# Optimization experiments

Measured on AMD Instinct MI355X. Metric: run time of the kernel, lower is better.

## Reference

```python
import jax, jax.numpy as jnp
import numpy as np

FCM_ITERS = 3
FCM_M = 2.0
EPS = 1e-8


def batched_index_select(x, idx):
    # x: [B, C, M, 1], idx: [B, N, K] -> [B, C, N, K]
    xt = x[..., 0]  # [B, C, M]
    return jnp.take_along_axis(xt[:, :, None, :], idx[:, None, :, :], axis=3)


def fcm_centroids(x, num_clusters):
    # Fuzzy c-means soft clustering (HyperedgeConstruction).
    # x: [B, C, N, 1] -> centroids [B, C, K], weights [B, N, 1, K]
    xt = jnp.transpose(x[..., 0], (0, 2, 1))  # [B, N, C]
    B, N, C = xt.shape
    init_idx = jnp.linspace(0, N - 1, num_clusters).astype(jnp.int32)
    cent = xt[:, init_idx, :]  # [B, K, C] deterministic init
    expo = -1.0 / (FCM_M - 1.0)

    def memberships(cent):
        xn = jnp.sum(xt * xt, axis=-1)            # [B, N]
        cn = jnp.sum(cent * cent, axis=-1)        # [B, K]
        d2 = xn[:, :, None] + cn[:, None, :] - 2.0 * jnp.einsum('bnc,bkc->bnk', xt, cent)
        d2 = jnp.maximum(d2, EPS)
        inv = d2 ** expo
        return inv / jnp.sum(inv, axis=-1, keepdims=True)  # [B, N, K]

    for _ in range(FCM_ITERS):
        u = memberships(cent)
        um = u ** FCM_M
        cent = jnp.einsum('bnk,bnc->bkc', um, xt) / (jnp.sum(um, axis=1)[..., None] + EPS)
    u = memberships(cent)
    centroids = jnp.transpose(cent, (0, 2, 1))  # [B, C, K]
    return centroids, u[:, :, None, :]          # weights [B, N, 1, K]


def setup_inputs() -> dict:
    key = jax.random.key(0)
    k1, k2, k3, k4 = jax.random.split(key, 4)
    B, C, N, K = 4, 64, 8192, 16
    OC = 64
    return {
        "x": jax.random.normal(k1, (B, C, N, 1), jnp.float32),
        "edge_index": jax.random.randint(k2, (2, B, N, K), 0, N),
        "W": jax.random.normal(k3, (OC, 3 * C), jnp.float32) / np.sqrt(3 * C).astype(np.float32),
        "b": jax.random.normal(k4, (OC,), jnp.float32) * 0.01,
        "num_clusters": 50,
        "top_clusters": 5,
    }


def reference(x, edge_index, W, b, num_clusters, top_clusters):
    B, C, N, _ = x.shape
    # max-relative neighbor feature
    x_i = batched_index_select(x, edge_index[1])          # [B, C, N, K]
    x_j = batched_index_select(x, edge_index[0])          # [B, C, N, K]
    x_j = jnp.max(x_j - x_i, axis=-1, keepdims=True)      # [B, C, N, 1]
    # soft-cluster (hyperedge) feature
    centroids, weights = fcm_centroids(x, num_clusters)   # [B,C,K], [B,N,1,K]
    weights = weights[:, :, 0, :]                         # squeeze(-2) -> [B, N, K]
    _, nn_idx_centroid = jax.lax.top_k(weights, top_clusters)  # [B, N, top]
    x_j_cluster = batched_index_select(centroids[..., None], nn_idx_centroid)  # [B, C, N, top]
    # x gathered at center_idx == x broadcast over top dim
    x_j_cluster = jnp.max(x_j_cluster - x, axis=-1, keepdims=True)  # [B, C, N, 1]
    # interleaved concat: [B, C, 3, N, 1] -> [B, 3C, N, 1]
    feat = jnp.stack([x, x_j, x_j_cluster], axis=2).reshape(B, 3 * C, N, 1)
    # BasicConv: 1x1 conv + ReLU
    out = jnp.einsum('oc,bcni->boni', W, feat) + b[None, :, None, None]
    return jax.nn.relu(out)
```

## Files before the change

kernel.cpp:

```cpp
#include <hip/hip_runtime.h>


constexpr int B  = 4;
constexpr int C  = 64;
constexpr int N  = 8192;
constexpr int KE = 16;
constexpr int OC = 64;
constexpr int NC = 50;
constexpr int TC = 5;
constexpr int C3 = 192;
constexpr int KG  = 5;
constexpr int NKG = 10;
constexpr int NS  = 8;
constexpr int MW  = 16;
constexpr float FEPS = 1e-8f;

__global__ __launch_bounds__(256) void k_transpose(const float* __restrict__ x,
                                                   float* __restrict__ xt,
                                                   float* __restrict__ xn) {
  __shared__ float tile[64][65];
  int b  = blockIdx.x >> 7;
  int n0 = (blockIdx.x & 127) << 6;
  int tid = threadIdx.x;
  int nl = tid & 63, cq = tid >> 6;
#pragma unroll
  for (int r = 0; r < 16; ++r) {
    int cc = r * 4 + cq;
    tile[cc][nl] = x[((size_t)b * C + cc) * N + n0 + nl];
  }
  __syncthreads();
  int cl = tid & 63, nq = tid >> 6;
#pragma unroll
  for (int r = 0; r < 16; ++r) {
    int nr = r * 4 + nq;
    xt[((size_t)b * N + n0 + nr) * C + cl] = tile[cl][nr];
  }
  if (tid < 64) {
    float s = 0.f;
#pragma unroll
    for (int cc = 0; cc < 64; ++cc) { float v = tile[cc][tid]; s = fmaf(v, v, s); }
    xn[(size_t)b * N + n0 + tid] = s;
  }
}

__global__ __launch_bounds__(256) void k_init(const float* __restrict__ xt,
                                              float* __restrict__ cent,
                                              float* __restrict__ cn) {
  int i = blockIdx.x * 256 + threadIdx.x;
  int lane = threadIdx.x & 63;
  int ccol = i & 63;
  int row  = i >> 6;
  int k = row % NC, b = row / NC;
  int src = (k * (N - 1)) / (NC - 1);
  float v = xt[((size_t)b * N + src) * C + ccol];
  cent[i] = v;
  float sq = v * v;
#pragma unroll
  for (int off = 32; off; off >>= 1) sq += __shfl_down(sq, off, 64);
  if (lane == 0) cn[row] = sq;
}

__global__ __launch_bounds__(512) void k_m1(const float* __restrict__ xt,
                                            const float* __restrict__ xn,
                                            const float* __restrict__ cent,
                                            const float* __restrict__ cn,
                                            float* __restrict__ umT) {
  int gid = blockIdx.x;
  int xcd = gid & 7;
  int b = xcd >> 1;
  int chunk = ((gid >> 3) << 1) + (xcd & 1);
  int n0 = chunk << 6;
  int w = __builtin_amdgcn_readfirstlane((int)threadIdx.x >> 6);
  int lane = threadIdx.x & 63;
  int n = n0 + lane;
  int base = (w < 2) ? 7 * w : 14 + 6 * (w - 2);
  int cnt  = (w < 2) ? 7 : 6;
  const float* xr = xt + ((size_t)b * N + n) * C;
  const float* cb = cent + b * NC * C;
  float dot[7];
#pragma unroll
  for (int j = 0; j < 7; ++j) dot[j] = 0.f;
  for (int c4 = 0; c4 < C; c4 += 4) {
    float4 xv = *(const float4*)(xr + c4);
#pragma unroll
    for (int j = 0; j < 7; ++j) {
      int kk = base + j; kk = (kk < NC) ? kk : 0;
      float4 cv = *(const float4*)(cb + kk * C + c4);
      dot[j] = fmaf(xv.x, cv.x, dot[j]);
      dot[j] = fmaf(xv.y, cv.y, dot[j]);
      dot[j] = fmaf(xv.z, cv.z, dot[j]);
      dot[j] = fmaf(xv.w, cv.w, dot[j]);
    }
  }
  float xnv = xn[(size_t)b * N + n];
  const float* cnb = cn + b * NC;
  float inv[7];
  float psum = 0.f;
#pragma unroll
  for (int j = 0; j < 7; ++j) {
    int kk = base + j; kk = (kk < NC) ? kk : 0;
    float d2 = fmaf(-2.f, dot[j], xnv + cnb[kk]);
    d2 = fmaxf(d2, FEPS);
    float iv = 1.f / d2;
    inv[j] = iv;
    psum += (j < cnt) ? iv : 0.f;
  }
  __shared__ float s_ps[8][64];
  s_ps[w][lane] = psum;
  __syncthreads();
  float ssum = 0.f;
#pragma unroll
  for (int ww = 0; ww < 8; ++ww) ssum += s_ps[ww][lane];
  float s2i = 1.f / (ssum * ssum);
  float* upT = umT + ((size_t)b * NC + base) * N + n;
#pragma unroll
  for (int j = 0; j < 7; ++j)
    if (j < cnt) upT[(size_t)j * N] = inv[j] * inv[j] * s2i;
}

__global__ __launch_bounds__(1024) void k_m2(const float* __restrict__ umT,
                                             const float* __restrict__ xt,
                                             float* __restrict__ part_c,
                                             float* __restrict__ part_u) {
  int gid = blockIdx.x;
  int xcd = gid & 7;
  int b = xcd >> 1;
  int r = ((gid >> 3) << 1) + (xcd & 1);
  int kg = r >> 3;
  int s  = r & 7;
  int k0 = kg * KG;
  int w = __builtin_amdgcn_readfirstlane((int)threadIdx.x >> 6);
  int c = threadIdx.x & 63;
  int sn0 = s * (N / NS);
  int nb = w * 64;
  const float* uT = umT + ((size_t)b * NC + k0) * N + sn0 + nb;
  const float* xb = xt + ((size_t)(b * N + sn0 + nb)) * C + c;
  float acc[KG], ua[KG];
#pragma unroll
  for (int j = 0; j < KG; ++j) { acc[j] = 0.f; ua[j] = 0.f; }
  for (int n4 = 0; n4 < 64; n4 += 4) {
    float4 u4[KG];
#pragma unroll
    for (int j = 0; j < KG; ++j)
      u4[j] = *(const float4*)(uT + (size_t)j * N + n4);
#pragma unroll
    for (int t = 0; t < 4; ++t) {
      float xv = xb[(size_t)(n4 + t) * C];
#pragma unroll
      for (int j = 0; j < KG; ++j) {
        float u = (t == 0) ? u4[j].x : (t == 1) ? u4[j].y : (t == 2) ? u4[j].z : u4[j].w;
        acc[j] = fmaf(u, xv, acc[j]);
        ua[j] += u;
      }
    }
  }
  __shared__ float s_acc[MW][KG][64];
  __shared__ float s_ua[MW][KG];
#pragma unroll
  for (int j = 0; j < KG; ++j) s_acc[w][j][c] = acc[j];
  if (c == 0) {
#pragma unroll
    for (int j = 0; j < KG; ++j) s_ua[w][j] = ua[j];
  }
  __syncthreads();
  if (w == 0) {
#pragma unroll
    for (int j = 0; j < KG; ++j) {
      float t = 0.f;
#pragma unroll
      for (int ww = 0; ww < MW; ++ww) t += s_acc[ww][j][c];
      part_c[((size_t)s * (B * NC) + b * NC + k0 + j) * C + c] = t;
    }
    if (c == 0) {
#pragma unroll
      for (int j = 0; j < KG; ++j) {
        float t = 0.f;
#pragma unroll
        for (int ww = 0; ww < MW; ++ww) t += s_ua[ww][j];
        part_u[(size_t)s * (B * NC) + b * NC + k0 + j] = t;
      }
    }
  }
}

__global__ __launch_bounds__(256) void k_m3(const float* __restrict__ part_c,
                                            const float* __restrict__ part_u,
                                            float* __restrict__ cent,
                                            float* __restrict__ cn) {
  int i = blockIdx.x * 256 + threadIdx.x;
  int lane = threadIdx.x & 63;
  int row = i >> 6;
  float tot = 0.f;
#pragma unroll
  for (int s = 0; s < NS; ++s) tot += part_c[(size_t)s * (B * NC * C) + i];
  float us = 0.f;
#pragma unroll
  for (int s = 0; s < NS; ++s) us += part_u[(size_t)s * (B * NC) + row];
  float v = tot / (us + FEPS);
  cent[i] = v;
  float sq = v * v;
#pragma unroll
  for (int off = 32; off; off >>= 1) sq += __shfl_down(sq, off, 64);
  if (lane == 0) cn[row] = sq;
}

__global__ __launch_bounds__(512) void k_top5(const float* __restrict__ xt,
                                              const float* __restrict__ xn,
                                              const float* __restrict__ cent,
                                              const float* __restrict__ cn,
                                              int* __restrict__ t5) {
  int gid = blockIdx.x;
  int xcd = gid & 7;
  int b = xcd >> 1;
  int chunk = ((gid >> 3) << 1) + (xcd & 1);
  int n0 = chunk << 6;
  int w = __builtin_amdgcn_readfirstlane((int)threadIdx.x >> 6);
  int lane = threadIdx.x & 63;
  int n = n0 + lane;
  int base = (w < 2) ? 7 * w : 14 + 6 * (w - 2);
  int cnt  = (w < 2) ? 7 : 6;
  const float* xr = xt + ((size_t)b * N + n) * C;
  const float* cb = cent + b * NC * C;
  float dot[7];
#pragma unroll
  for (int j = 0; j < 7; ++j) dot[j] = 0.f;
  for (int c4 = 0; c4 < C; c4 += 4) {
    float4 xv = *(const float4*)(xr + c4);
#pragma unroll
    for (int j = 0; j < 7; ++j) {
      int kk = base + j; kk = (kk < NC) ? kk : 0;
      float4 cv = *(const float4*)(cb + kk * C + c4);
      dot[j] = fmaf(xv.x, cv.x, dot[j]);
      dot[j] = fmaf(xv.y, cv.y, dot[j]);
      dot[j] = fmaf(xv.z, cv.z, dot[j]);
      dot[j] = fmaf(xv.w, cv.w, dot[j]);
    }
  }
  float xnv = xn[(size_t)b * N + n];
  const float* cnb = cn + b * NC;
  __shared__ float s_inv[NC][65];
#pragma unroll
  for (int j = 0; j < 7; ++j) {
    int kk = base + j; kk = (kk < NC) ? kk : 0;
    float d2 = fmaxf(fmaf(-2.f, dot[j], xnv + cnb[kk]), FEPS);
    float iv = 1.f / d2;
    if (j < cnt) s_inv[base + j][lane] = iv;
  }
  __syncthreads();
  if (w == 0) {
    float v[NC];
#pragma unroll
    for (int k = 0; k < NC; ++k) v[k] = s_inv[k][lane];
    unsigned long long taken = 0ull;
    int* tp = t5 + ((size_t)b * N + n) * TC;
#pragma unroll
    for (int t = 0; t < TC; ++t) {
      float best = -1.f;
      int bi = 0;
#pragma unroll
      for (int k = 0; k < NC; ++k) {
        bool ok = (((taken >> k) & 1ull) == 0ull) && (v[k] > best);
        best = ok ? v[k] : best;
        bi   = ok ? k : bi;
      }
      taken |= (1ull << bi);
      tp[t] = bi;
    }
  }
}

__global__ __launch_bounds__(512, 4) void k_out(const float* __restrict__ xt,
                                                const float* __restrict__ cent,
                                                const float* __restrict__ W,
                                                const int* __restrict__ t5,
                                                const int* __restrict__ eidx,
                                                const float* __restrict__ bias,
                                                float* __restrict__ out) {
  __shared__ float s_feat[C3][65];
  int tid = threadIdx.x;
  int gid = blockIdx.x;
  int xcd = gid & 7;
  int b = xcd >> 1;
  int chunk = ((gid >> 3) << 1) + (xcd & 1);
  int wv = __builtin_amdgcn_readfirstlane(tid >> 6);
  int lane = tid & 63;
  int n0 = chunk * 64;
  int nw0 = n0 + wv * 8;
  const float* xtb = xt + ((size_t)b * N) * C;
  const float* cb  = cent + b * NC * C;
  const int* e0b = eidx + ((size_t)b * N) * KE;
  const int* e1b = eidx + ((size_t)(B + b) * N) * KE;
  int c = lane;
  int fr = wv * 8;
#pragma unroll
  for (int j = 0; j < 8; ++j) {
    int n = nw0 + j;
    const int* p0 = e0b + (size_t)n * KE;
    const int* p1 = e1b + (size_t)n * KE;
    const int* tp = t5 + ((size_t)b * N + n) * TC;
    float x0 = xtb[(size_t)n * C + c];
    float g0[KE], g1[KE];
#pragma unroll
    for (int k = 0; k < KE; ++k) {
      g0[k] = xtb[(size_t)p0[k] * C + c];
      g1[k] = xtb[(size_t)p1[k] * C + c];
    }
    float cv[TC];
#pragma unroll
    for (int t = 0; t < TC; ++t) cv[t] = cb[(size_t)tp[t] * C + c];
    float m1 = g0[0] - g1[0];
#pragma unroll
    for (int k = 1; k < KE; ++k) m1 = fmaxf(m1, g0[k] - g1[k]);
    float cm = cv[0];
#pragma unroll
    for (int t = 1; t < TC; ++t) cm = fmaxf(cm, cv[t]);
    s_feat[3 * c + 0][fr + j] = x0;
    s_feat[3 * c + 1][fr + j] = m1;
    s_feat[3 * c + 2][fr + j] = cm - x0;
  }
  __syncthreads();
  int o0 = wv * 8;
  float acc[8];
#pragma unroll
  for (int oj = 0; oj < 8; ++oj) acc[oj] = bias[o0 + oj];
#pragma unroll 4
  for (int f = 0; f < C3; ++f) {
    float v = s_feat[f][lane];
#pragma unroll
    for (int oj = 0; oj < 8; ++oj)
      acc[oj] = fmaf(W[(size_t)(o0 + oj) * C3 + f], v, acc[oj]);
  }
  float* ob = out + ((size_t)b * OC + o0) * N + n0 + lane;
#pragma unroll
  for (int oj = 0; oj < 8; ++oj)
    ob[(size_t)oj * N] = fmaxf(acc[oj], 0.f);
}

extern "C" void kernel_launch(void* const* d_in, const int* in_sizes, int n_in,
                              void* d_out, int out_size, void* d_ws, size_t ws_size,
                              hipStream_t stream) {
  const float* x    = (const float*)d_in[0];
  const int*   eidx = (const int*)d_in[1];
  const float* W    = (const float*)d_in[2];
  const float* bias = (const float*)d_in[3];

  float* ws   = (float*)d_ws;
  float* xt   = ws;
  float* xn   = xt + (size_t)B * N * C;
  float* cent = xn + (size_t)B * N;
  float* cn   = cent + B * NC * C;
  float* umT  = cn + 256;
  float* pc   = umT + (size_t)B * NC * N;
  float* pu   = pc + (size_t)NS * B * NC * C;
  int*   t5   = (int*)(pu + NS * B * NC);
  float* out  = (float*)d_out;

  k_transpose<<<dim3(B * (N / 64)), dim3(256), 0, stream>>>(x, xt, xn);
  k_init<<<dim3((B * NC * C) / 256), dim3(256), 0, stream>>>(xt, cent, cn);
  for (int it = 0; it < 3; ++it) {
    k_m1<<<dim3(512), dim3(512), 0, stream>>>(xt, xn, cent, cn, umT);
    k_m2<<<dim3(B * NKG * NS), dim3(1024), 0, stream>>>(umT, xt, pc, pu);
    k_m3<<<dim3((B * NC * C) / 256), dim3(256), 0, stream>>>(pc, pu, cent, cn);
  }
  k_top5<<<dim3(512), dim3(512), 0, stream>>>(xt, xn, cent, cn, t5);
  k_out<<<dim3(512), dim3(512), 0, stream>>>(xt, cent, W, t5, eidx, bias, out);
}
```

Before: 240.9 us.

## Fuse FCM membership and centroid partial-sum kernels via shared memory

Merges the membership kernel and the centroid accumulation kernel into one kernel per iteration. Each block keeps its 64-point slice of features and the membership values in shared memory and writes per-chunk partial centroid sums directly. This removes the global write and re-read of the B×NC×N membership matrix and one launch per iteration. In exchange the final reduction kernel now sums 128 partial slices instead of 8, and the accumulation loop reads shared memory with possible bank conflicts.

```diff
diff --git a/kernel.cpp b/kernel.cpp
--- a/kernel.cpp
+++ b/kernel.cpp
@@ -9,10 +9,7 @@
 constexpr int NC = 50;
 constexpr int TC = 5;
 constexpr int C3 = 192;
-constexpr int KG  = 5;
-constexpr int NKG = 10;
-constexpr int NS  = 8;
-constexpr int MW  = 16;
+constexpr int NSL = 128;
 constexpr float FEPS = 1e-8f;
 
 __global__ __launch_bounds__(256) void k_transpose(const float* __restrict__ x,
@@ -60,11 +57,15 @@
   if (lane == 0) cn[row] = sq;
 }
 
-__global__ __launch_bounds__(512) void k_m1(const float* __restrict__ xt,
-                                            const float* __restrict__ xn,
-                                            const float* __restrict__ cent,
-                                            const float* __restrict__ cn,
-                                            float* __restrict__ umT) {
+__global__ __launch_bounds__(512) void k_fcm(const float* __restrict__ xt,
+                                             const float* __restrict__ xn,
+                                             const float* __restrict__ cent,
+                                             const float* __restrict__ cn,
+                                             float* __restrict__ pc,
+                                             float* __restrict__ pu) {
+  __shared__ float s_xt[64][68];
+  __shared__ float s_u[NC][64];
+  __shared__ float s_ps[8][64];
   int gid = blockIdx.x;
   int xcd = gid & 7;
   int b = xcd >> 1;
@@ -82,6 +83,7 @@
   for (int j = 0; j < 7; ++j) dot[j] = 0.f;
   for (int c4 = 0; c4 < C; c4 += 4) {
     float4 xv = *(const float4*)(xr + c4);
+    if (w == 0) *(float4*)(&s_xt[lane][c4]) = xv;
 #pragma unroll
     for (int j = 0; j < 7; ++j) {
       int kk = base + j; kk = (kk < NC) ? kk : 0;
@@ -105,97 +107,54 @@
     inv[j] = iv;
     psum += (j < cnt) ? iv : 0.f;
   }
-  __shared__ float s_ps[8][64];
   s_ps[w][lane] = psum;
   __syncthreads();
   float ssum = 0.f;
 #pragma unroll
   for (int ww = 0; ww < 8; ++ww) ssum += s_ps[ww][lane];
   float s2i = 1.f / (ssum * ssum);
-  float* upT = umT + ((size_t)b * NC + base) * N + n;
 #pragma unroll
   for (int j = 0; j < 7; ++j)
-    if (j < cnt) upT[(size_t)j * N] = inv[j] * inv[j] * s2i;
-}
-
-__global__ __launch_bounds__(1024) void k_m2(const float* __restrict__ umT,
-                                             const float* __restrict__ xt,
-                                             float* __restrict__ part_c,
-                                             float* __restrict__ part_u) {
-  int gid = blockIdx.x;
-  int xcd = gid & 7;
-  int b = xcd >> 1;
-  int r = ((gid >> 3) << 1) + (xcd & 1);
-  int kg = r >> 3;
-  int s  = r & 7;
-  int k0 = kg * KG;
-  int w = __builtin_amdgcn_readfirstlane((int)threadIdx.x >> 6);
-  int c = threadIdx.x & 63;
-  int sn0 = s * (N / NS);
-  int nb = w * 64;
-  const float* uT = umT + ((size_t)b * NC + k0) * N + sn0 + nb;
-  const float* xb = xt + ((size_t)(b * N + sn0 + nb)) * C + c;
-  float acc[KG], ua[KG];
-#pragma unroll
-  for (int j = 0; j < KG; ++j) { acc[j] = 0.f; ua[j] = 0.f; }
-  for (int n4 = 0; n4 < 64; n4 += 4) {
-    float4 u4[KG];
-#pragma unroll
-    for (int j = 0; j < KG; ++j)
-      u4[j] = *(const float4*)(uT + (size_t)j * N + n4);
-#pragma unroll
-    for (int t = 0; t < 4; ++t) {
-      float xv = xb[(size_t)(n4 + t) * C];
-#pragma unroll
-      for (int j = 0; j < KG; ++j) {
-        float u = (t == 0) ? u4[j].x : (t == 1) ? u4[j].y : (t == 2) ? u4[j].z : u4[j].w;
-        acc[j] = fmaf(u, xv, acc[j]);
-        ua[j] += u;
-      }
-    }
-  }
-  __shared__ float s_acc[MW][KG][64];
-  __shared__ float s_ua[MW][KG];
-#pragma unroll
-  for (int j = 0; j < KG; ++j) s_acc[w][j][c] = acc[j];
-  if (c == 0) {
-#pragma unroll
-    for (int j = 0; j < KG; ++j) s_ua[w][j] = ua[j];
-  }
-  __syncthreads();
-  if (w == 0) {
-#pragma unroll
-    for (int j = 0; j < KG; ++j) {
-      float t = 0.f;
-#pragma unroll
-      for (int ww = 0; ww < MW; ++ww) t += s_acc[ww][j][c];
-      part_c[((size_t)s * (B * NC) + b * NC + k0 + j) * C + c] = t;
-    }
-    if (c == 0) {
-#pragma unroll
-      for (int j = 0; j < KG; ++j) {
-        float t = 0.f;
-#pragma unroll
-        for (int ww = 0; ww < MW; ++ww) t += s_ua[ww][j];
-        part_u[(size_t)s * (B * NC) + b * NC + k0 + j] = t;
-      }
-    }
-  }
-}
-
-__global__ __launch_bounds__(256) void k_m3(const float* __restrict__ part_c,
-                                            const float* __restrict__ part_u,
+    if (j < cnt) s_u[base + j][lane] = inv[j] * inv[j] * s2i;
+  __syncthreads();
+  int c = lane;
+  float acc[7], ua[7];
+#pragma unroll
+  for (int j = 0; j < 7; ++j) { acc[j] = 0.f; ua[j] = 0.f; }
+  for (int nn = 0; nn < 64; ++nn) {
+    float xv = s_xt[nn][c];
+#pragma unroll
+    for (int j = 0; j < 7; ++j) {
+      int kk = base + j; kk = (kk < NC) ? kk : 0;
+      float u = s_u[kk][nn];
+      acc[j] = fmaf(u, xv, acc[j]);
+      ua[j] += u;
+    }
+  }
+  float* pcb = pc + (((size_t)chunk * (B * NC) + b * NC + base)) * C + c;
+#pragma unroll
+  for (int j = 0; j < 7; ++j)
+    if (j < cnt) pcb[(size_t)j * C] = acc[j];
+  if (lane == 0) {
+#pragma unroll
+    for (int j = 0; j < 7; ++j)
+      if (j < cnt) pu[(size_t)chunk * (B * NC) + b * NC + base + j] = ua[j];
+  }
+}
+
+__global__ __launch_bounds__(256) void k_m3(const float* __restrict__ pc,
+                                            const float* __restrict__ pu,
                                             float* __restrict__ cent,
                                             float* __restrict__ cn) {
   int i = blockIdx.x * 256 + threadIdx.x;
   int lane = threadIdx.x & 63;
   int row = i >> 6;
   float tot = 0.f;
-#pragma unroll
-  for (int s = 0; s < NS; ++s) tot += part_c[(size_t)s * (B * NC * C) + i];
+#pragma unroll 16
+  for (int s = 0; s < NSL; ++s) tot += pc[(size_t)s * (B * NC * C) + i];
   float us = 0.f;
-#pragma unroll
-  for (int s = 0; s < NS; ++s) us += part_u[(size_t)s * (B * NC) + row];
+#pragma unroll 16
+  for (int s = 0; s < NSL; ++s) us += pu[(size_t)s * (B * NC) + row];
   float v = tot / (us + FEPS);
   cent[i] = v;
   float sq = v * v;
@@ -349,17 +308,15 @@
   float* xn   = xt + (size_t)B * N * C;
   float* cent = xn + (size_t)B * N;
   float* cn   = cent + B * NC * C;
-  float* umT  = cn + 256;
-  float* pc   = umT + (size_t)B * NC * N;
-  float* pu   = pc + (size_t)NS * B * NC * C;
-  int*   t5   = (int*)(pu + NS * B * NC);
+  float* pc   = cn + 256;
+  float* pu   = pc + (size_t)NSL * B * NC * C;
+  int*   t5   = (int*)(pu + (size_t)NSL * B * NC);
   float* out  = (float*)d_out;
 
   k_transpose<<<dim3(B * (N / 64)), dim3(256), 0, stream>>>(x, xt, xn);
   k_init<<<dim3((B * NC * C) / 256), dim3(256), 0, stream>>>(xt, cent, cn);
   for (int it = 0; it < 3; ++it) {
-    k_m1<<<dim3(512), dim3(512), 0, stream>>>(xt, xn, cent, cn, umT);
-    k_m2<<<dim3(B * NKG * NS), dim3(1024), 0, stream>>>(umT, xt, pc, pu);
+    k_fcm<<<dim3(512), dim3(512), 0, stream>>>(xt, xn, cent, cn, pc, pu);
     k_m3<<<dim3((B * NC * C) / 256), dim3(256), 0, stream>>>(pc, pu, cent, cn);
   }
   k_top5<<<dim3(512), dim3(512), 0, stream>>>(xt, xn, cent, cn, t5);
```

New measurement: 232.9 us. 1.03x faster.
